# Kernel tuning notes

Measured on AMD Instinct MI355X. Metric: run time of the kernel, lower is better.

The kernel has to match this reference:

```python
import jax, jax.numpy as jnp
import numpy as np

TAU_EPS = 1e-6
T_SCALAR = 1.0  # call() default t when given a single tensor
NUM_HEADS = 8


def setup_inputs() -> dict:
    key = jax.random.key(0)
    ks = jax.random.split(key, 12)
    B, T, dm = 4, 1024, 512
    ph, th = 64, 32  # phi hidden, tau hidden
    pd = 128         # 2 * depth (pairwise concat dim per head)

    def w(k, shape):
        return jax.random.normal(k, shape, jnp.float32) / jnp.sqrt(jnp.float32(shape[0]))

    return {
        "x": jax.random.normal(ks[0], (B, T, dm), jnp.float32),
        "Wq": w(ks[1], (dm, dm)), "bq": jnp.zeros((dm,), jnp.float32),
        "Wk": w(ks[2], (dm, dm)), "bk": jnp.zeros((dm,), jnp.float32),
        "Wv": w(ks[3], (dm, dm)), "bv": jnp.zeros((dm,), jnp.float32),
        "Wphi_in": w(ks[4], (pd, ph)), "bphi_in": jnp.zeros((ph,), jnp.float32),
        "Wphi_out": w(ks[5], (ph, 1)), "bphi_out": jnp.zeros((1,), jnp.float32),
        "Wta": w(ks[6], (pd, 1)), "bta": jnp.zeros((1,), jnp.float32),
        "Wtb": w(ks[7], (pd, 1)), "btb": jnp.zeros((1,), jnp.float32),
        "Wtau_in": w(ks[8], (pd, th)), "btau_in": jnp.zeros((th,), jnp.float32),
        "Wtau_out": w(ks[9], (th, 1)), "btau_out": jnp.zeros((1,), jnp.float32),
        "Wo": w(ks[10], (dm, dm)), "bo": jnp.zeros((dm,), jnp.float32),
    }


def _lan_forward(x, Wq, bq, Wk, bk, Wv, bv,
                 Wphi_in, bphi_in, Wphi_out, bphi_out,
                 Wta, bta, Wtb, btb,
                 Wtau_in, btau_in, Wtau_out, btau_out,
                 Wo, bo):
    B, T, dm = x.shape
    H = NUM_HEADS
    D = dm // H

    def heads(z):  # [B,T,dm] -> [B,H,T,D]
        return z.reshape(B, T, H, D).transpose(0, 2, 1, 3)

    q = heads(x @ Wq + bq)
    k = heads(x @ Wk + bk)
    v = heads(x @ Wv + bv)

    # phi_in/phi_out, tau_in/tau_out, time_a, time_b are all linear Dense
    # layers acting on concat([q_i, k_j]) (dim 2D). A linear map on a concat
    # equals (per-q scalar) + (per-k scalar) + bias, so fold the two-layer
    # linear stacks into a single [2D] vector and broadcast-add -- exact math,
    # no [B,H,T,T,2D] materialization.
    def pair_scalar(w2d, b0):  # w2d: [2D], b0: scalar -> [B,H,Tq,Tk]
        sq = jnp.einsum('bhtd,d->bht', q, w2d[:D])
        sk = jnp.einsum('bhtd,d->bht', k, w2d[D:])
        return sq[..., :, None] + sk[..., None, :] + b0

    w_phi = (Wphi_in @ Wphi_out)[:, 0]
    b_phi = bphi_in @ Wphi_out[:, 0] + bphi_out[0]
    phi = jax.nn.sigmoid(pair_scalar(w_phi, b_phi))

    t_a = pair_scalar(Wta[:, 0], bta[0])
    t_b = pair_scalar(Wtb[:, 0], btb[0])
    t_interp = jax.nn.sigmoid(t_a * T_SCALAR + t_b)

    w_tau = (Wtau_in @ Wtau_out)[:, 0]
    b_tau = btau_in @ Wtau_out[:, 0] + btau_out[0]
    tau = jax.nn.softplus(pair_scalar(w_tau, b_tau)) + TAU_EPS

    # mode == 'exact': a(t) = (phi/tau) * (1 - exp(-tau * t))
    attn_logits = phi / tau * (1.0 - jnp.exp(-tau * t_interp))
    attn = jax.nn.softmax(attn_logits, axis=-1)

    out = jnp.einsum('bhqk,bhkd->bhqd', attn, v)          # [B,H,T,D]
    out = out.transpose(0, 2, 1, 3).reshape(B, T, dm)      # combine heads
    return out @ Wo + bo                                   # return_sequences=True, linear activation


def reference(x, Wq, bq, Wk, bk, Wv, bv,
              Wphi_in, bphi_in, Wphi_out, bphi_out,
              Wta, bta, Wtb, btb,
              Wtau_in, btau_in, Wtau_out, btau_out,
              Wo, bo):
    return _lan_forward(x, Wq, bq, Wk, bk, Wv, bv,
                        Wphi_in, bphi_in, Wphi_out, bphi_out,
                        Wta, bta, Wtb, btb,
                        Wtau_in, btau_in, Wtau_out, btau_out,
                        Wo, bo)
```

## Files before the change

kernel.cpp:

```cpp
#include <hip/hip_runtime.h>
#include <hip/hip_bf16.h>

#define B_  4
#define T_  1024
#define H_  8
#define NTOK (B_*T_)

#define CONST_OFF 512
#define UTH_OFF   576
#define UTL_OFF   12864
#define XHI_OFF   25152
#define XLO_OFF   1073728
#define WVTH_OFF  2122304
#define WVTL_OFF  2253376
#define WOTH_OFF  2384448
#define WOTL_OFF  2515520
#define S_OFF     2646592
#define VT_OFF    2843200

#define LOG2E 1.4426950408889634f
#define LN2SQ 0.4804530139182014f

typedef __attribute__((ext_vector_type(4))) float v4f;
typedef __attribute__((ext_vector_type(8))) short v8s;

__device__ inline short bf16r(float f) {
  union { float f; unsigned u; } v; v.f = f;
  return (short)((v.u + 0x7FFFu + ((v.u >> 16) & 1u)) >> 16);
}
__device__ inline float bf16f(short s) {
  union { unsigned u; float f; } v; v.u = ((unsigned)(unsigned short)s) << 16; return v.f;
}
__device__ inline unsigned cvt_pk_bf16(float lo, float hi) {
  unsigned r;
  asm("v_cvt_pk_bf16_f32 %0, %1, %2" : "=v"(r) : "v"(lo), "v"(hi));
  return r;
}

__global__ __launch_bounds__(256) void k_prep(
    const float* __restrict__ Wphi_in, const float* __restrict__ Wphi_out,
    const float* __restrict__ bphi_in, const float* __restrict__ bphi_out,
    const float* __restrict__ Wta, const float* __restrict__ bta,
    const float* __restrict__ Wtb, const float* __restrict__ btb,
    const float* __restrict__ Wtau_in, const float* __restrict__ Wtau_out,
    const float* __restrict__ btau_in, const float* __restrict__ btau_out,
    const float* __restrict__ Wq, const float* __restrict__ bq,
    const float* __restrict__ Wk, const float* __restrict__ bk,
    const float* __restrict__ x, const float* __restrict__ Wv, const float* __restrict__ Wo,
    short* __restrict__ Uth, short* __restrict__ Utl, float* __restrict__ consts,
    short* __restrict__ xh, short* __restrict__ xl,
    short* __restrict__ Wvh, short* __restrict__ Wvl,
    short* __restrict__ Woh, short* __restrict__ Wol) {
  __shared__ float wv[390];
  __shared__ float tile[64][65];
  int bx = blockIdx.x, t = threadIdx.x;
  if (bx < 96) {
    if (t < 128) {
      float wp = 0.f;
      for (int j = 0; j < 64; ++j) wp += Wphi_in[t*64+j] * Wphi_out[j];
      float wt = 0.f;
      for (int j = 0; j < 32; ++j) wt += Wtau_in[t*32+j] * Wtau_out[j];
      wv[t]       = wp;
      wv[128 + t] = Wta[t] + Wtb[t];
      wv[256 + t] = wt;
    } else if (t == 128) {
      float bp = bphi_out[0];
      for (int j = 0; j < 64; ++j) bp += bphi_in[j]*Wphi_out[j];
      float bt = btau_out[0];
      for (int j = 0; j < 32; ++j) bt += btau_in[j]*Wtau_out[j];
      wv[384] = bp;
      wv[385] = bta[0] + btb[0];
      wv[386] = bt;
    }
    __syncthreads();
    int idx = bx*256 + t;
    int c = idx & 511;
    int s = idx >> 9;
    int h = s / 6, tt = s % 6;
    int qk = tt / 3;
    int which = tt % 3;
    float scale = (which == 2) ? LOG2E : -LOG2E;
    const float* W = qk ? Wk : Wq;
    const float* wvec = wv + which*128 + qk*64;
    const float* row = W + c*512 + h*64;
    float acc = 0.f;
    #pragma unroll 8
    for (int d = 0; d < 64; ++d) acc += row[d] * wvec[d];
    float v = acc * scale;
    short hi = bf16r(v);
    Uth[s*512 + c] = hi;
    Utl[s*512 + c] = bf16r(v - bf16f(hi));
    if (c == 0) {
      const float* bb = qk ? bk : bq;
      float cs = 0.f;
      for (int d = 0; d < 64; ++d) cs += bb[h*64+d] * wvec[d];
      if (qk == 0) cs += wv[384 + which];
      consts[s] = cs * scale;
    }
    return;
  }
  if (bx < 1120) {
    size_t i = (size_t)((bx-96)*256 + t) * 8;
    float4 a = *(const float4*)(x + i);
    float4 b = *(const float4*)(x + i + 4);
    float vals[8] = {a.x,a.y,a.z,a.w,b.x,b.y,b.z,b.w};
    v8s hi, lo;
    #pragma unroll
    for (int j = 0; j < 8; ++j) {
      short h = bf16r(vals[j]);
      hi[j] = h;
      lo[j] = bf16r(vals[j] - bf16f(h));
    }
    *(v8s*)(xh + i) = hi;
    *(v8s*)(xl + i) = lo;
    return;
  }
  int idx = bx - 1120;
  int z = idx >> 6, rem = idx & 63;
  int k0 = (rem >> 3)*64, n0 = (rem & 7)*64;
  const float* src = z ? Wo : Wv;
  short* dh = z ? Woh : Wvh;
  short* dl = z ? Wol : Wvl;
  int kr = t >> 2, cq = t & 3;
  #pragma unroll
  for (int i = 0; i < 4; ++i) {
    float4 v = *(const float4*)(src + (size_t)(k0+kr)*512 + n0 + cq*16 + i*4);
    tile[kr][cq*16+i*4+0] = v.x; tile[kr][cq*16+i*4+1] = v.y;
    tile[kr][cq*16+i*4+2] = v.z; tile[kr][cq*16+i*4+3] = v.w;
  }
  __syncthreads();
  int nr = t >> 2, ko = t & 3;
  v8s h0,h1,l0,l1;
  #pragma unroll
  for (int i = 0; i < 8; ++i) {
    float a = tile[ko*16+i][nr];
    float b = tile[ko*16+8+i][nr];
    short ha = bf16r(a), hb = bf16r(b);
    h0[i] = ha; l0[i] = bf16r(a - bf16f(ha));
    h1[i] = hb; l1[i] = bf16r(b - bf16f(hb));
  }
  size_t base = (size_t)(n0+nr)*512 + k0 + ko*16;
  *(v8s*)(dh + base) = h0; *(v8s*)(dh + base + 8) = h1;
  *(v8s*)(dl + base) = l0; *(v8s*)(dl + base + 8) = l1;
}

template<int MODE>
__device__ __forceinline__ void gemm_body(char* smem, int mb, int nb,
    const short* __restrict__ Ah, const short* __restrict__ Al,
    const short* __restrict__ Bh, const short* __restrict__ Bl,
    const float* __restrict__ bias, float* __restrict__ C, short* __restrict__ VT) {
  short (*As_h)[40] = (short(*)[40])(smem);
  short (*As_l)[40] = (short(*)[40])(smem + 5120);
  short (*Bs_h)[40] = (short(*)[40])(smem + 10240);
  short (*Bs_l)[40] = (short(*)[40])(smem + 15360);
  int tid = threadIdx.x, l = tid & 63, ra = l & 15, kg = l >> 4;
  int w = tid >> 6, wr = w >> 1, wc = w & 1;
  v4f acc[2][2] = {};
  int srow = tid >> 2, soct = tid & 3;
  const short* gAh = Ah + (size_t)(mb*64+srow)*512 + soct*8;
  const short* gAl = Al + (size_t)(mb*64+srow)*512 + soct*8;
  const short* gBh = Bh + (size_t)(nb*64+srow)*512 + soct*8;
  const short* gBl = Bl + (size_t)(nb*64+srow)*512 + soct*8;
  v8s sa = *(const v8s*)(gAh);
  v8s sb = *(const v8s*)(gAl);
  v8s sc = *(const v8s*)(gBh);
  v8s sd = *(const v8s*)(gBl);
  for (int k0 = 0; k0 < 512; k0 += 32) {
    __syncthreads();
    *(v8s*)&As_h[srow][soct*8] = sa;
    *(v8s*)&As_l[srow][soct*8] = sb;
    *(v8s*)&Bs_h[srow][soct*8] = sc;
    *(v8s*)&Bs_l[srow][soct*8] = sd;
    if (k0 < 480) {
      sa = *(const v8s*)(gAh + k0 + 32);
      sb = *(const v8s*)(gAl + k0 + 32);
      sc = *(const v8s*)(gBh + k0 + 32);
      sd = *(const v8s*)(gBl + k0 + 32);
    }
    __syncthreads();
    v8s ah[2], al[2], bh[2], bl[2];
    #pragma unroll
    for (int mi = 0; mi < 2; ++mi) {
      int r = wr*32 + mi*16 + ra;
      ah[mi] = *(const v8s*)&As_h[r][kg*8];
      al[mi] = *(const v8s*)&As_l[r][kg*8];
    }
    #pragma unroll
    for (int ni = 0; ni < 2; ++ni) {
      int r = wc*32 + ni*16 + ra;
      bh[ni] = *(const v8s*)&Bs_h[r][kg*8];
      bl[ni] = *(const v8s*)&Bs_l[r][kg*8];
    }
    #pragma unroll
    for (int mi = 0; mi < 2; ++mi)
      #pragma unroll
      for (int ni = 0; ni < 2; ++ni) {
        acc[mi][ni] = __builtin_amdgcn_mfma_f32_16x16x32_bf16(ah[mi], bh[ni], acc[mi][ni], 0, 0, 0);
        acc[mi][ni] = __builtin_amdgcn_mfma_f32_16x16x32_bf16(ah[mi], bl[ni], acc[mi][ni], 0, 0, 0);
        acc[mi][ni] = __builtin_amdgcn_mfma_f32_16x16x32_bf16(al[mi], bh[ni], acc[mi][ni], 0, 0, 0);
      }
  }
  if constexpr (MODE == 0) {
    #pragma unroll
    for (int ni = 0; ni < 2; ++ni) {
      int n = nb*64 + wc*32 + ni*16 + ra;
      float bv_ = bias[n];
      #pragma unroll
      for (int mi = 0; mi < 2; ++mi) {
        int row = mb*64 + wr*32 + mi*16 + kg*4;
        #pragma unroll
        for (int r = 0; r < 4; ++r)
          C[(size_t)(row+r)*512 + n] = acc[mi][ni][r] + bv_;
      }
    }
  } else {
    __syncthreads();
    float (*ldsT)[65] = (float(*)[65])(smem);
    #pragma unroll
    for (int ni = 0; ni < 2; ++ni) {
      int lc = wc*32 + ni*16 + ra;
      float bv_ = bias[nb*64 + lc];
      #pragma unroll
      for (int mi = 0; mi < 2; ++mi) {
        int lr = wr*32 + mi*16 + kg*4;
        #pragma unroll
        for (int r = 0; r < 4; ++r)
          ldsT[lc][lr+r] = acc[mi][ni][r] + bv_;
      }
    }
    __syncthreads();
    int d = tid >> 2, tq = tid & 3;
    v8s h0, h1;
    #pragma unroll
    for (int i = 0; i < 8; ++i) {
      h0[i] = bf16r(ldsT[d][tq*16+i]);
      h1[i] = bf16r(ldsT[d][tq*16+8+i]);
    }
    size_t base = ((size_t)(((mb>>4)*8 + nb)*64 + d))*1024 + (mb&15)*64 + tq*16;
    *(v8s*)(VT + base)     = h0;
    *(v8s*)(VT + base + 8) = h1;
  }
}

__device__ __forceinline__ void S_body(char* smem, int mb,
    const short* __restrict__ xh, const short* __restrict__ xl,
    const short* __restrict__ Uth, const short* __restrict__ Utl,
    const float* __restrict__ consts, float* __restrict__ E) {
  float* red = (float*)smem;
  int tid = threadIdx.x, w = tid >> 6, l = tid & 63, ra = l & 15, kg = l >> 4;
  v4f acc[3] = {{0,0,0,0},{0,0,0,0},{0,0,0,0}};
  const short* xa = xh + (size_t)(mb*16+ra)*512;
  const short* xb = xl + (size_t)(mb*16+ra)*512;
  #pragma unroll
  for (int ks = 0; ks < 4; ++ks) {
    int kk = w*128 + ks*32 + kg*8;
    v8s ah = *(const v8s*)(xa + kk);
    v8s al = *(const v8s*)(xb + kk);
    #pragma unroll
    for (int nf = 0; nf < 3; ++nf) {
      v8s bh = *(const v8s*)(Uth + (size_t)(nf*16+ra)*512 + kk);
      v8s bl = *(const v8s*)(Utl + (size_t)(nf*16+ra)*512 + kk);
      acc[nf] = __builtin_amdgcn_mfma_f32_16x16x32_bf16(ah, bh, acc[nf], 0, 0, 0);
      acc[nf] = __builtin_amdgcn_mfma_f32_16x16x32_bf16(ah, bl, acc[nf], 0, 0, 0);
      acc[nf] = __builtin_amdgcn_mfma_f32_16x16x32_bf16(al, bh, acc[nf], 0, 0, 0);
    }
  }
  if (w > 0) {
    #pragma unroll
    for (int nf = 0; nf < 3; ++nf) *(v4f*)(red + ((w-1)*64 + l)*12 + nf*4) = acc[nf];
  }
  __syncthreads();
  if (w == 0) {
    #pragma unroll
    for (int p = 0; p < 3; ++p)
      #pragma unroll
      for (int nf = 0; nf < 3; ++nf) acc[nf] += *(const v4f*)(red + (p*64 + l)*12 + nf*4);
    int t0 = mb*16 + kg*4;
    #pragma unroll
    for (int nf = 0; nf < 3; ++nf) {
      int s = nf*16 + ra;
      float cns = consts[s];
      v4f o;
      #pragma unroll
      for (int c = 0; c < 4; ++c) o[c] = __builtin_amdgcn_exp2f(acc[nf][c] + cns);
      *(v4f*)(E + (size_t)s*NTOK + t0) = o;
    }
  }
}

__global__ __launch_bounds__(256) void k_mid(
    const short* __restrict__ xh, const short* __restrict__ xl,
    const short* __restrict__ Uth, const short* __restrict__ Utl,
    const float* __restrict__ consts, float* __restrict__ E,
    const short* __restrict__ Wvh, const short* __restrict__ Wvl,
    const float* __restrict__ bv, short* __restrict__ VT) {
  __shared__ __align__(16) char smem[20480];
  int bx = blockIdx.x;
  if (bx < 256) {
    S_body(smem, bx, xh, xl, Uth, Utl, consts, E);
  } else {
    int i = bx - 256;
    gemm_body<1>(smem, i >> 3, i & 7, xh, xl, Wvh, Wvl, bv, nullptr, VT);
  }
}

__global__ __launch_bounds__(256) void k_out(
    const short* __restrict__ Ah, const short* __restrict__ Al,
    const short* __restrict__ Bh, const short* __restrict__ Bl,
    const float* __restrict__ bias, float* __restrict__ C) {
  __shared__ __align__(16) char smem[20480];
  gemm_body<0>(smem, blockIdx.x, blockIdx.y, Ah, Al, Bh, Bl, bias, C, nullptr);
}

__global__ __launch_bounds__(256) void k_attn(const float* __restrict__ E,
                                              const short* __restrict__ VT,
                                              short* __restrict__ AOh, short* __restrict__ AOl) {
  __shared__ float red[3][64][40];
  int tid = threadIdx.x, w = tid >> 6, l = tid & 63, ra = l & 15, kg = l >> 4;
  int bh = blockIdx.y, b = bh >> 3, h = bh & 7;
  int q0 = blockIdx.x * 32;
  const float* Eb = E + (size_t)h*6*NTOK + b*T_;
  float eqp[2], eqc[2], eqt[2];
  #pragma unroll
  for (int ai = 0; ai < 2; ++ai) {
    eqp[ai] = Eb[q0 + ai*16 + ra];
    eqc[ai] = Eb[NTOK + q0 + ai*16 + ra];
    eqt[ai] = Eb[2*NTOK + q0 + ai*16 + ra];
  }
  const float* Ekp = Eb + 3*NTOK;
  const float* Ekc = Eb + 4*NTOK;
  const float* Ekt = Eb + 5*NTOK;
  const short* Vb = VT + (size_t)bh*64*1024 + (size_t)ra*1024;

  v4f acc[2][4] = {};
  v4f dacc[2] = {};
  v8s ones;
  #pragma unroll
  for (int j = 0; j < 8; ++j) ones[j] = (short)0x3F80;

  #pragma unroll 2
  for (int ks = 0; ks < 8; ++ks) {
    int kk = w*256 + ks*32 + kg*8;
    v4f p0 = *(const v4f*)&Ekp[kk], p1 = *(const v4f*)&Ekp[kk+4];
    v4f c0 = *(const v4f*)&Ekc[kk], c1 = *(const v4f*)&Ekc[kk+4];
    v4f t0 = *(const v4f*)&Ekt[kk], t1 = *(const v4f*)&Ekt[kk+4];
    v8s bfr[4];
    #pragma unroll
    for (int ni = 0; ni < 4; ++ni) bfr[ni] = *(const v8s*)(Vb + (size_t)ni*16*1024 + kk);
    #pragma unroll
    for (int ai = 0; ai < 2; ++ai) {
      float p8[8];
      #pragma unroll
      for (int j = 0; j < 8; ++j) {
        float Ep = (j < 4) ? p0[j] : p1[j-4];
        float Ec = (j < 4) ? c0[j] : c1[j-4];
        float Et = (j < 4) ? t0[j] : t1[j-4];
        float ephi = eqp[ai] * Ep;
        float ec   = eqc[ai] * Ec;
        float g    = eqt[ai] * Et;
        float ti   = __builtin_amdgcn_rcpf(1.f + ec);
        float t2   = __builtin_amdgcn_logf(1.f + g);
        float z    = 1.f - __builtin_amdgcn_exp2f(-t2 * ti);
        float den  = (1.f + ephi) * fmaf(t2, LN2SQ, 6.93e-7f);
        p8[j] = __builtin_amdgcn_exp2f(z * __builtin_amdgcn_rcpf(den));
      }
      union { unsigned u[4]; v8s s; } af;
      af.u[0] = cvt_pk_bf16(p8[0], p8[1]);
      af.u[1] = cvt_pk_bf16(p8[2], p8[3]);
      af.u[2] = cvt_pk_bf16(p8[4], p8[5]);
      af.u[3] = cvt_pk_bf16(p8[6], p8[7]);
      v8s afrag = af.s;
      #pragma unroll
      for (int ni = 0; ni < 4; ++ni)
        acc[ai][ni] = __builtin_amdgcn_mfma_f32_16x16x32_bf16(afrag, bfr[ni], acc[ai][ni], 0, 0, 0);
      dacc[ai] = __builtin_amdgcn_mfma_f32_16x16x32_bf16(afrag, ones, dacc[ai], 0, 0, 0);
    }
  }

  if (w > 0) {
    float* rp = &red[w-1][l][0];
    #pragma unroll
    for (int ai = 0; ai < 2; ++ai) {
      #pragma unroll
      for (int ni = 0; ni < 4; ++ni) *(v4f*)(rp + ai*16 + ni*4) = acc[ai][ni];
      *(v4f*)(rp + 32 + ai*4) = dacc[ai];
    }
  }
  __syncthreads();
  if (w == 0) {
    #pragma unroll
    for (int p = 0; p < 3; ++p) {
      const float* rp = &red[p][l][0];
      #pragma unroll
      for (int ai = 0; ai < 2; ++ai) {
        #pragma unroll
        for (int ni = 0; ni < 4; ++ni) acc[ai][ni] += *(const v4f*)(rp + ai*16 + ni*4);
        dacc[ai] += *(const v4f*)(rp + 32 + ai*4);
      }
    }
    #pragma unroll
    for (int ai = 0; ai < 2; ++ai) {
      size_t qb = (size_t)(b*T_ + q0 + ai*16 + kg*4);
      #pragma unroll
      for (int r = 0; r < 4; ++r) {
        float inv = __builtin_amdgcn_rcpf(dacc[ai][r]);
        size_t o = (qb + r)*512 + h*64 + ra;
        #pragma unroll
        for (int ni = 0; ni < 4; ++ni) {
          float v = acc[ai][ni][r] * inv;
          short hh = bf16r(v);
          AOh[o + ni*16] = hh;
          AOl[o + ni*16] = bf16r(v - bf16f(hh));
        }
      }
    }
  }
}

extern "C" void kernel_launch(void* const* d_in, const int* in_sizes, int n_in,
                              void* d_out, int out_size, void* d_ws, size_t ws_size,
                              hipStream_t stream) {
  (void)in_sizes; (void)n_in; (void)out_size; (void)ws_size;
  const float* x        = (const float*)d_in[0];
  const float* Wq       = (const float*)d_in[1];
  const float* bq       = (const float*)d_in[2];
  const float* Wk       = (const float*)d_in[3];
  const float* bk       = (const float*)d_in[4];
  const float* Wv       = (const float*)d_in[5];
  const float* bv       = (const float*)d_in[6];
  const float* Wphi_in  = (const float*)d_in[7];
  const float* bphi_in  = (const float*)d_in[8];
  const float* Wphi_out = (const float*)d_in[9];
  const float* bphi_out = (const float*)d_in[10];
  const float* Wta      = (const float*)d_in[11];
  const float* bta      = (const float*)d_in[12];
  const float* Wtb      = (const float*)d_in[13];
  const float* btb      = (const float*)d_in[14];
  const float* Wtau_in  = (const float*)d_in[15];
  const float* btau_in  = (const float*)d_in[16];
  const float* Wtau_out = (const float*)d_in[17];
  const float* btau_out = (const float*)d_in[18];
  const float* Wo       = (const float*)d_in[19];
  const float* bo       = (const float*)d_in[20];
  float* out = (float*)d_out;
  float* ws  = (float*)d_ws;

  float* consts = ws + CONST_OFF;
  short* Uth    = (short*)(ws + UTH_OFF);
  short* Utl    = (short*)(ws + UTL_OFF);
  short* xhi    = (short*)(ws + XHI_OFF);
  short* xlo    = (short*)(ws + XLO_OFF);
  short* AOh    = (short*)(ws + XHI_OFF);
  short* AOl    = (short*)(ws + XLO_OFF);
  short* Wvth   = (short*)(ws + WVTH_OFF);
  short* Wvtl   = (short*)(ws + WVTL_OFF);
  short* Woth   = (short*)(ws + WOTH_OFF);
  short* Wotl   = (short*)(ws + WOTL_OFF);
  float* E      = ws + S_OFF;
  short* VT     = (short*)(ws + VT_OFF);

  hipLaunchKernelGGL(k_prep, dim3(1248), dim3(256), 0, stream,
                     Wphi_in, Wphi_out, bphi_in, bphi_out, Wta, bta, Wtb, btb,
                     Wtau_in, Wtau_out, btau_in, btau_out,
                     Wq, bq, Wk, bk, x, Wv, Wo,
                     Uth, Utl, consts, xhi, xlo, Wvth, Wvtl, Woth, Wotl);
  hipLaunchKernelGGL(k_mid, dim3(768), dim3(256), 0, stream,
                     xhi, xlo, Uth, Utl, consts, E, Wvth, Wvtl, bv, VT);
  hipLaunchKernelGGL(k_attn, dim3(T_/32, B_*H_), dim3(256), 0, stream, E, VT, AOh, AOl);
  hipLaunchKernelGGL(k_out, dim3(NTOK/64, 8), dim3(256), 0, stream,
                     AOh, AOl, Woth, Wotl, bo, out);
}
```

Before: 69.56 us.

## Drop low-half A operand in split-bf16 GEMMs and load fragments directly from global

Measured after the change: 90.80 us. +30.5%, slower.

```diff
diff --git a/kernel.cpp b/kernel.cpp
--- a/kernel.cpp
+++ b/kernel.cpp
@@ -146,59 +146,31 @@
 
 template<int MODE>
 __device__ __forceinline__ void gemm_body(char* smem, int mb, int nb,
-    const short* __restrict__ Ah, const short* __restrict__ Al,
+    const short* __restrict__ Ah,
     const short* __restrict__ Bh, const short* __restrict__ Bl,
     const float* __restrict__ bias, float* __restrict__ C, short* __restrict__ VT) {
-  short (*As_h)[40] = (short(*)[40])(smem);
-  short (*As_l)[40] = (short(*)[40])(smem + 5120);
-  short (*Bs_h)[40] = (short(*)[40])(smem + 10240);
-  short (*Bs_l)[40] = (short(*)[40])(smem + 15360);
   int tid = threadIdx.x, l = tid & 63, ra = l & 15, kg = l >> 4;
   int w = tid >> 6, wr = w >> 1, wc = w & 1;
   v4f acc[2][2] = {};
-  int srow = tid >> 2, soct = tid & 3;
-  const short* gAh = Ah + (size_t)(mb*64+srow)*512 + soct*8;
-  const short* gAl = Al + (size_t)(mb*64+srow)*512 + soct*8;
-  const short* gBh = Bh + (size_t)(nb*64+srow)*512 + soct*8;
-  const short* gBl = Bl + (size_t)(nb*64+srow)*512 + soct*8;
-  v8s sa = *(const v8s*)(gAh);
-  v8s sb = *(const v8s*)(gAl);
-  v8s sc = *(const v8s*)(gBh);
-  v8s sd = *(const v8s*)(gBl);
+  const short* gA  = Ah + (size_t)(mb*64 + wr*32 + ra)*512 + kg*8;
+  const short* gBh = Bh + (size_t)(nb*64 + wc*32 + ra)*512 + kg*8;
+  const short* gBl = Bl + (size_t)(nb*64 + wc*32 + ra)*512 + kg*8;
+  #pragma unroll 4
   for (int k0 = 0; k0 < 512; k0 += 32) {
-    __syncthreads();
-    *(v8s*)&As_h[srow][soct*8] = sa;
-    *(v8s*)&As_l[srow][soct*8] = sb;
-    *(v8s*)&Bs_h[srow][soct*8] = sc;
-    *(v8s*)&Bs_l[srow][soct*8] = sd;
-    if (k0 < 480) {
-      sa = *(const v8s*)(gAh + k0 + 32);
-      sb = *(const v8s*)(gAl + k0 + 32);
-      sc = *(const v8s*)(gBh + k0 + 32);
-      sd = *(const v8s*)(gBl + k0 + 32);
-    }
-    __syncthreads();
-    v8s ah[2], al[2], bh[2], bl[2];
-    #pragma unroll
-    for (int mi = 0; mi < 2; ++mi) {
-      int r = wr*32 + mi*16 + ra;
-      ah[mi] = *(const v8s*)&As_h[r][kg*8];
-      al[mi] = *(const v8s*)&As_l[r][kg*8];
-    }
-    #pragma unroll
-    for (int ni = 0; ni < 2; ++ni) {
-      int r = wc*32 + ni*16 + ra;
-      bh[ni] = *(const v8s*)&Bs_h[r][kg*8];
-      bl[ni] = *(const v8s*)&Bs_l[r][kg*8];
-    }
-    #pragma unroll
-    for (int mi = 0; mi < 2; ++mi)
-      #pragma unroll
-      for (int ni = 0; ni < 2; ++ni) {
-        acc[mi][ni] = __builtin_amdgcn_mfma_f32_16x16x32_bf16(ah[mi], bh[ni], acc[mi][ni], 0, 0, 0);
-        acc[mi][ni] = __builtin_amdgcn_mfma_f32_16x16x32_bf16(ah[mi], bl[ni], acc[mi][ni], 0, 0, 0);
-        acc[mi][ni] = __builtin_amdgcn_mfma_f32_16x16x32_bf16(al[mi], bh[ni], acc[mi][ni], 0, 0, 0);
-      }
+    v8s a0  = *(const v8s*)(gA + k0);
+    v8s a1  = *(const v8s*)(gA + 16*512 + k0);
+    v8s b0h = *(const v8s*)(gBh + k0);
+    v8s b1h = *(const v8s*)(gBh + 16*512 + k0);
+    v8s b0l = *(const v8s*)(gBl + k0);
+    v8s b1l = *(const v8s*)(gBl + 16*512 + k0);
+    acc[0][0] = __builtin_amdgcn_mfma_f32_16x16x32_bf16(a0, b0h, acc[0][0], 0, 0, 0);
+    acc[0][0] = __builtin_amdgcn_mfma_f32_16x16x32_bf16(a0, b0l, acc[0][0], 0, 0, 0);
+    acc[0][1] = __builtin_amdgcn_mfma_f32_16x16x32_bf16(a0, b1h, acc[0][1], 0, 0, 0);
+    acc[0][1] = __builtin_amdgcn_mfma_f32_16x16x32_bf16(a0, b1l, acc[0][1], 0, 0, 0);
+    acc[1][0] = __builtin_amdgcn_mfma_f32_16x16x32_bf16(a1, b0h, acc[1][0], 0, 0, 0);
+    acc[1][0] = __builtin_amdgcn_mfma_f32_16x16x32_bf16(a1, b0l, acc[1][0], 0, 0, 0);
+    acc[1][1] = __builtin_amdgcn_mfma_f32_16x16x32_bf16(a1, b1h, acc[1][1], 0, 0, 0);
+    acc[1][1] = __builtin_amdgcn_mfma_f32_16x16x32_bf16(a1, b1l, acc[1][1], 0, 0, 0);
   }
   if constexpr (MODE == 0) {
     #pragma unroll
@@ -214,7 +186,6 @@
       }
     }
   } else {
-    __syncthreads();
     float (*ldsT)[65] = (float(*)[65])(smem);
     #pragma unroll
     for (int ni = 0; ni < 2; ++ni) {
@@ -294,27 +265,26 @@
     const float* __restrict__ consts, float* __restrict__ E,
     const short* __restrict__ Wvh, const short* __restrict__ Wvl,
     const float* __restrict__ bv, short* __restrict__ VT) {
-  __shared__ __align__(16) char smem[20480];
+  __shared__ __align__(16) char smem[16640];
   int bx = blockIdx.x;
   if (bx < 256) {
     S_body(smem, bx, xh, xl, Uth, Utl, consts, E);
   } else {
     int i = bx - 256;
-    gemm_body<1>(smem, i >> 3, i & 7, xh, xl, Wvh, Wvl, bv, nullptr, VT);
+    gemm_body<1>(smem, i >> 3, i & 7, xh, Wvh, Wvl, bv, nullptr, VT);
   }
 }
 
 __global__ __launch_bounds__(256) void k_out(
-    const short* __restrict__ Ah, const short* __restrict__ Al,
+    const short* __restrict__ Ah,
     const short* __restrict__ Bh, const short* __restrict__ Bl,
     const float* __restrict__ bias, float* __restrict__ C) {
-  __shared__ __align__(16) char smem[20480];
-  gemm_body<0>(smem, blockIdx.x, blockIdx.y, Ah, Al, Bh, Bl, bias, C, nullptr);
+  gemm_body<0>(nullptr, blockIdx.x, blockIdx.y, Ah, Bh, Bl, bias, C, nullptr);
 }
 
 __global__ __launch_bounds__(256) void k_attn(const float* __restrict__ E,
                                               const short* __restrict__ VT,
-                                              short* __restrict__ AOh, short* __restrict__ AOl) {
+                                              short* __restrict__ AOh) {
   __shared__ float red[3][64][40];
   int tid = threadIdx.x, w = tid >> 6, l = tid & 63, ra = l & 15, kg = l >> 4;
   int bh = blockIdx.y, b = bh >> 3, h = bh & 7;
@@ -406,12 +376,8 @@
         float inv = __builtin_amdgcn_rcpf(dacc[ai][r]);
         size_t o = (qb + r)*512 + h*64 + ra;
         #pragma unroll
-        for (int ni = 0; ni < 4; ++ni) {
-          float v = acc[ai][ni][r] * inv;
-          short hh = bf16r(v);
-          AOh[o + ni*16] = hh;
-          AOl[o + ni*16] = bf16r(v - bf16f(hh));
-        }
+        for (int ni = 0; ni < 4; ++ni)
+          AOh[o + ni*16] = bf16r(acc[ai][ni][r] * inv);
       }
     }
   }
@@ -451,7 +417,6 @@
   short* xhi    = (short*)(ws + XHI_OFF);
   short* xlo    = (short*)(ws + XLO_OFF);
   short* AOh    = (short*)(ws + XHI_OFF);
-  short* AOl    = (short*)(ws + XLO_OFF);
   short* Wvth   = (short*)(ws + WVTH_OFF);
   short* Wvtl   = (short*)(ws + WVTL_OFF);
   short* Woth   = (short*)(ws + WOTH_OFF);
@@ -466,7 +431,7 @@
                      Uth, Utl, consts, xhi, xlo, Wvth, Wvtl, Woth, Wotl);
   hipLaunchKernelGGL(k_mid, dim3(768), dim3(256), 0, stream,
                      xhi, xlo, Uth, Utl, consts, E, Wvth, Wvtl, bv, VT);
-  hipLaunchKernelGGL(k_attn, dim3(T_/32, B_*H_), dim3(256), 0, stream, E, VT, AOh, AOl);
+  hipLaunchKernelGGL(k_attn, dim3(T_/32, B_*H_), dim3(256), 0, stream, E, VT, AOh);
   hipLaunchKernelGGL(k_out, dim3(NTOK/64, 8), dim3(256), 0, stream,
-                     AOh, AOl, Woth, Wotl, bo, out);
-}
+                     AOh, Woth, Wotl, bo, out);
+}
```
